# Performance work log

Hardware: AMD Instinct MI355X
Metric: run time of the kernel (lower is better)

The kernel has to match this reference:

```python
import jax, jax.numpy as jnp
import numpy as np

# SSD prior config (small VGGLite-style)
FEATURE_MAPS = [10, 5, 3, 1]
BOXES_PER_LOC = [4, 4, 4, 4]
IMG = 128      # ssd_config.DATA.SHAPE[0] -> WhereTransformer image_size
OBJ = 64
ZWHAT = 64
HID = 512
B = 4
N_OBJ = sum(f * f for f in FEATURE_MAPS)                       # 135
N_FEAT = sum(b * f * f for f, b in zip(FEATURE_MAPS, BOXES_PER_LOC))  # 540


def reconstruction_indices():
    # Replicates Decoder.reconstruction_indices: map per-location latents to per-box slots.
    idx = []
    last = 0
    for f, bpl in zip(FEATURE_MAPS, BOXES_PER_LOC):
        for i in range(f * f):
            idx.extend([last + i] * bpl)
        last += f * f
    return np.asarray(idx, dtype=np.int32)


def what_decode(z, W1, b1, W2, b2):
    # WhatDecoder: MLP z_what -> 3xOBJxOBJ object glyph in (0,1)
    h = jax.nn.relu(z @ W1 + b1)
    return jax.nn.sigmoid(h @ W2 + b2).reshape(-1, 3, OBJ, OBJ)


def where_stn(imgs, zw):
    # WhereTransformer: paste each object image into its (cx, cy, w, h) box on an IMGxIMG canvas
    # via inverse-affine bilinear sampling with zero padding (STN / grid_sample semantics).
    cx, cy, w, h = zw[:, 0], zw[:, 1], zw[:, 2], zw[:, 3]
    w = jnp.maximum(w, 1e-2)
    h = jnp.maximum(h, 1e-2)
    lin = jnp.linspace(-1.0, 1.0, IMG)
    gy, gx = jnp.meshgrid(lin, lin, indexing='ij')           # (IMG, IMG)
    u = (gx[None] - (2.0 * cx - 1.0)[:, None, None]) / w[:, None, None]
    v = (gy[None] - (2.0 * cy - 1.0)[:, None, None]) / h[:, None, None]
    px = (u + 1.0) * 0.5 * (OBJ - 1)                          # (N, IMG, IMG)
    py = (v + 1.0) * 0.5 * (OBJ - 1)

    def sample_one(img, py, px):  # img: (3, OBJ, OBJ)
        x0 = jnp.floor(px); y0 = jnp.floor(py)
        wx = px - x0; wy = py - y0
        x0i = x0.astype(jnp.int32); y0i = y0.astype(jnp.int32)

        def tap(yi, xi, wgt):
            valid = (yi >= 0) & (yi < OBJ) & (xi >= 0) & (xi < OBJ)
            yc = jnp.clip(yi, 0, OBJ - 1)
            xc = jnp.clip(xi, 0, OBJ - 1)
            return img[:, yc, xc] * (wgt * valid)[None]

        return (tap(y0i, x0i, (1 - wy) * (1 - wx)) + tap(y0i, x0i + 1, (1 - wy) * wx)
                + tap(y0i + 1, x0i, wy * (1 - wx)) + tap(y0i + 1, x0i + 1, wy * wx))

    return jax.vmap(sample_one)(imgs, py, px)                 # (N, 3, IMG, IMG)


def setup_inputs() -> dict:
    key = jax.random.key(0)
    ks = jax.random.split(key, 8)
    return {
        'z_what': jax.random.normal(ks[0], (B, N_OBJ, ZWHAT), jnp.float32),
        'z_where': jax.random.uniform(ks[1], (B, N_FEAT, 4), jnp.float32),
        'z_depth': jax.random.normal(ks[2], (B, N_OBJ, 1), jnp.float32),
        'W1': jax.random.normal(ks[3], (ZWHAT, HID), jnp.float32) * 0.05,
        'b1': jnp.zeros((HID,), jnp.float32),
        'W2': jax.random.normal(ks[4], (HID, 3 * OBJ * OBJ), jnp.float32) * 0.02,
        'b2': jnp.zeros((3 * OBJ * OBJ,), jnp.float32),
        'z_present': jax.random.randint(ks[5], (B, N_FEAT, 1), 0, 2, jnp.int32),
    }


def reference(z_what, z_where, z_depth, W1, b1, W2, b2, z_present):
    idx = jnp.asarray(reconstruction_indices())
    # index_select: replicate per-location latents across boxes-per-location
    zw_full = z_what[:, idx]                                  # (B, N_FEAT, ZWHAT)
    zd_full = z_depth[:, idx]                                 # (B, N_FEAT, 1)
    # sort descending by depth; gather all latents in that order
    order = jnp.argsort(-zd_full[..., 0], axis=1)             # (B, N_FEAT)
    s_what = jnp.take_along_axis(zw_full, order[..., None], axis=1)
    s_where = jnp.take_along_axis(z_where, order[..., None], axis=1)
    s_pres = jnp.take_along_axis(z_present, order[..., None], axis=1)
    # decode + STN warp all objects; absent objects are zeroed (equivalent to the
    dec = what_decode(s_what.reshape(-1, ZWHAT), W1, b1, W2, b2)
    warped = where_stn(dec, s_where.reshape(-1, 4))
    imgs = warped.reshape(B, N_FEAT, 3, IMG, IMG) * s_pres.astype(warped.dtype)[..., None, None]
    # depth compositing: per channel-pixel, take the first nonzero value in sorted order
    nz = imgs != 0
    first = jnp.argmax(nz, axis=1)                            # (B, 3, IMG, IMG)
    out = jnp.take_along_axis(imgs, first[:, None], axis=1)[:, 0] * nz.any(axis=1)
    return out
```

## Files before the change

### kernel.cpp

```cpp
#include <hip/hip_runtime.h>
#include <hip/hip_bf16.h>
#include <math.h>

#define NBOX  540
#define NOBJ  135
#define ZW    64
#define HIDN  512
#define NOUT  12288
#define OBJS  64
#define BATCH 4

#define ROLE_WIN   256
#define ROLE_G1    540
#define PRE_BLOCKS (ROLE_WIN + ROLE_G1)

#define G2_BLOCKS  1920

#define OFF_NROWS  0u
#define OFF_USED   256u
#define OFF_REMAP  2560u
#define OFF_ROWOBJ 4864u
#define OFF_PXWIN  7680u
#define OFF_HBF    269824u
#define OFF_DEC    13508096u

typedef short  bf16x8 __attribute__((ext_vector_type(8)));
typedef float  f32x4  __attribute__((ext_vector_type(4)));

struct F4 { float x, y, z, w; };

#define GLOAD_LDS16(gp, lp)                                                    \
  __builtin_amdgcn_global_load_lds(                                            \
      (const __attribute__((address_space(1))) void*)(gp),                     \
      (__attribute__((address_space(3))) void*)(lp), 16, 0, 0)

__device__ __forceinline__ unsigned short f2bf(float x) {
  __hip_bfloat16 h = __float2bfloat16(x);
  return *(unsigned short*)&h;
}

__global__ __launch_bounds__(256) void k_pre(
    const float* __restrict__ z_depth,
    const float* __restrict__ z_where,
    const int*   __restrict__ z_present,
    const float* __restrict__ Z,
    const float* __restrict__ W1,
    const float* __restrict__ b1,
    int* __restrict__ nrowsp,
    int* __restrict__ used,
    int* __restrict__ remap,
    int* __restrict__ rowobj,
    int* __restrict__ pxwin,
    unsigned short* __restrict__ Hbf)
{
  __shared__ union ShMem {
    struct {
      unsigned long long keys[256];
      F4       cf[NBOX];
      unsigned cbb[NBOX];
      int      cbx[NBOX];
    } win;
    float    zs[ZW];
  } u;
  __shared__ int wsums[4], woff[4], nPs;

  const int bid = blockIdx.x;
  const int t   = threadIdx.x;

  if (bid < ROLE_WIN) {
#pragma clang fp contract(off)
    const int b    = bid >> 6;
    const int tile = bid & 63;
    const int lane = t & 63, wv = t >> 6;
    const int y = (tile >> 3) * 16 + (t >> 4);
    const int x = (tile & 7) * 16 + (t & 15);

    unsigned long long key = ~0ull;
    if (t < NOBJ) {
      unsigned uu = __float_as_uint(z_depth[b * NOBJ + t]);
      uu = (uu & 0x80000000u) ? ~uu : (uu | 0x80000000u);
      key = ((unsigned long long)(~uu) << 32) | (unsigned)t;
    }
    u.win.keys[t] = key;
    __syncthreads();
    for (int k = 2; k <= 256; k <<= 1) {
      for (int j = k >> 1; j > 0; j >>= 1) {
        int ixj = t ^ j;
        if (ixj > t) {
          unsigned long long a = u.win.keys[t], c = u.win.keys[ixj];
          bool asc = (t & k) == 0;
          if (asc ? (a > c) : (a < c)) { u.win.keys[t] = c; u.win.keys[ixj] = a; }
        }
        __syncthreads();
      }
    }

    int boxq[3], presq[3], cnt = 0;
#pragma unroll
    for (int q = 0; q < 3; q++) {
      int e = 3 * t + q;
      presq[q] = 0; boxq[q] = 0;
      if (e < NBOX) {
        int o  = (int)(u.win.keys[e >> 2] & 0xFFFFFFFFull);
        int bx = o * 4 + (e & 3);
        boxq[q]  = bx;
        presq[q] = (z_present[b * NBOX + bx] != 0) ? 1 : 0;
        cnt += presq[q];
      }
    }
    int incl = cnt;
#pragma unroll
    for (int o = 1; o < 64; o <<= 1) {
      int vprev = __shfl_up(incl, o, 64);
      if (lane >= o) incl += vprev;
    }
    if (lane == 63) wsums[wv] = incl;
    __syncthreads();
    if (t == 0) {
      int a = 0;
#pragma unroll
      for (int i = 0; i < 4; i++) { woff[i] = a; a += wsums[i]; }
      nPs = a;
    }
    __syncthreads();
    int slot = woff[wv] + incl - cnt;
#pragma unroll
    for (int q = 0; q < 3; q++) {
      if (presq[q]) {
        int bx = boxq[q];
        F4 p = *(const F4*)&z_where[((size_t)b * NBOX + bx) * 4];
        double w  = fmax((double)p.z, 0.01);
        double h  = fmax((double)p.w, 0.01);
        double tx = 2.0 * (double)p.x - 1.0;
        double ty = 2.0 * (double)p.y - 1.0;
        const double S = 65.0 / 63.0;
        int xlo = (int)floor((tx - w * S + 1.0) * 63.5) - 1;
        int xhi = (int)floor((tx + w * S + 1.0) * 63.5) + 2;
        int ylo = (int)floor((ty - h * S + 1.0) * 63.5) - 1;
        int yhi = (int)floor((ty + h * S + 1.0) * 63.5) + 2;
        xlo = max(xlo, 0); ylo = max(ylo, 0);
        xhi = min(xhi, 127); yhi = min(yhi, 127);
        unsigned bb = (xhi < xlo || yhi < ylo) ? 0xFFu
                    : ((unsigned)xlo | ((unsigned)xhi << 8) |
                       ((unsigned)ylo << 16) | ((unsigned)yhi << 24));
        F4 f;
        f.x = (float)tx; f.y = (float)ty;
        f.z = (float)(w * S); f.w = (float)(h * S);
        u.win.cf[slot]  = f;
        u.win.cbb[slot] = bb;
        u.win.cbx[slot] = bx;
        slot++;
      }
    }
    __syncthreads();

    const int nP = nPs;
    const double step = 2.0 / 127.0;
    const double gx = (x == 127) ? 1.0 : ((double)x * step + (-1.0));
    const double gy = (y == 127) ? 1.0 : ((double)y * step + (-1.0));
    const float gxf = (float)gx, gyf = (float)gy;
    const int tx0 = (tile & 7) * 16, tx1 = tx0 + 15;
    const int wy0 = (tile >> 3) * 16 + wv * 4, wy1 = wy0 + 3;

    bool done = false;
    int  win  = -1;
    for (int j = 0; j < nP; j++) {
      if (__all((int)done)) break;
      unsigned bb = u.win.cbb[j];
      int bxlo = (int)(bb & 255u),         bxhi = (int)((bb >> 8) & 255u);
      int bylo = (int)((bb >> 16) & 255u), byhi = (int)(bb >> 24);
      if (bxhi < tx0 || bxlo > tx1 || byhi < wy0 || bylo > wy1) continue;
      bool newly = false;
      if (!done) {
        F4 f = u.win.cf[j];
        float dx = fabsf(gxf - f.x), dy = fabsf(gyf - f.y);
        bool in_lo = (dx < f.z * 0.9999f - 2e-6f) & (dy < f.w * 0.9999f - 2e-6f);
        bool in_hi = (dx < f.z * 1.0001f + 2e-6f) & (dy < f.w * 1.0001f + 2e-6f);
        bool cov;
        if (in_lo) {
          cov = true;
        } else if (!in_hi) {
          cov = false;
        } else {
          F4 p = *(const F4*)&z_where[((size_t)b * NBOX + u.win.cbx[j]) * 4];
          double w  = fmax((double)p.z, 0.01);
          double h  = fmax((double)p.w, 0.01);
          double tx = 2.0 * (double)p.x - 1.0;
          double ty = 2.0 * (double)p.y - 1.0;
          double uu = (gx - tx) / w;
          double vv = (gy - ty) / h;
          double px = (uu + 1.0) * 0.5 * 63.0;
          double py = (vv + 1.0) * 0.5 * 63.0;
          cov = (px > -1.0) && (px < 64.0) && (py > -1.0) && (py < 64.0);
        }
        if (cov) { win = u.win.cbx[j]; done = true; newly = true; }
      }
      unsigned long long nm = __ballot((int)newly);
      if (nm != 0ull && lane == (int)__builtin_ctzll(nm)) {
        int oi = b * NOBJ + (win >> 2);
        if (atomicCAS(&used[oi], 0, 1) == 0) {
          int rr = atomicAdd(nrowsp, 1);
          rowobj[rr] = oi;
          remap[oi]  = rr;
        }
      }
    }
    pxwin[b * 16384 + y * 128 + x] = win;
  } else {
    const int r = bid - ROLE_WIN;
    if (t < ZW) u.zs[t] = Z[(size_t)r * ZW + t];
    __syncthreads();
    float a0 = b1[t], a1 = b1[t + 256];
#pragma unroll 8
    for (int k = 0; k < ZW; k++) {
      float z = u.zs[k];
      a0 += z * W1[(size_t)k * HIDN + t];
      a1 += z * W1[(size_t)k * HIDN + t + 256];
    }
    Hbf[(size_t)r * HIDN + t]       = f2bf(fmaxf(a0, 0.f));
    Hbf[(size_t)r * HIDN + t + 256] = f2bf(fmaxf(a1, 0.f));
  }
}

__global__ __launch_bounds__(256) void k_gemm2_mfma(
    const unsigned short* __restrict__ Hbf,
    const float* __restrict__ W2,
    const float* __restrict__ b2,
    const int* __restrict__ nrowsp,
    const int* __restrict__ rowobj,
    float* __restrict__ dec)
{
  __shared__ unsigned short As[2][128 * 32];
  __shared__ float          BsF[2][32 * 32];
  const int nr = *nrowsp;
  int bid = (int)blockIdx.x;
  bid = (bid & 7) * 240 + (bid >> 3);
  const int m0 = (bid % 5) * 128;
  if (m0 >= nr) return;
  const int n0 = (bid / 5) * 32;

  const int t    = threadIdx.x;
  const int lane = t & 63, wv = t >> 6;
  const int wm = (wv & 1) * 64;
  const int wn = (wv >> 1) * 16;

  const int r0  = t >> 2;
  const int kc0 = (t & 3) ^ (r0 & 3);
  const int r1  = r0 + 64;
  const int kc1 = (t & 3) ^ (r1 & 3);

  const int ga0 = (m0 + r0 < nr) ? rowobj[m0 + r0] : 0;
  const int ga1 = (m0 + r1 < nr) ? rowobj[m0 + r1] : 0;
  const unsigned short* a0p = Hbf + (size_t)ga0 * HIDN + kc0 * 8;
  const unsigned short* a1p = Hbf + (size_t)ga1 * HIDN + kc1 * 8;
  const float* bp = W2 + (size_t)(t >> 3) * NOUT + n0 + (t & 7) * 4;

  const int fr = lane & 15;
  const int fj = lane >> 4;
  f32x4 acc[4] = {};

#define STAGE(buf, kt)                                                         \
  do {                                                                         \
    GLOAD_LDS16(a0p + (kt) * 32, &As[buf][t * 8]);                             \
    GLOAD_LDS16(a1p + (kt) * 32, &As[buf][(t + 256) * 8]);                     \
    GLOAD_LDS16(bp + (size_t)(kt) * 32 * NOUT, &BsF[buf][t * 4]);              \
  } while (0)

  STAGE(0, 0);
  __syncthreads();
  int cur = 0;
  for (int kt = 0; kt < HIDN / 32; ++kt) {
    if (kt < HIDN / 32 - 1) STAGE(cur ^ 1, kt + 1);
    bf16x8 av[4];
#pragma unroll
    for (int mi = 0; mi < 4; mi++) {
      int row = wm + mi * 16 + fr;
      av[mi] = *(const bf16x8*)&As[cur][(row * 4 + (fj ^ (row & 3))) * 8];
    }
    bf16x8 bv;
#pragma unroll
    for (int j = 0; j < 8; j++)
      bv[j] = (short)f2bf(BsF[cur][(fj * 8 + j) * 32 + wn + fr]);
#pragma unroll
    for (int mi = 0; mi < 4; mi++)
      acc[mi] = __builtin_amdgcn_mfma_f32_16x16x32_bf16(av[mi], bv, acc[mi], 0, 0, 0);
    __syncthreads();
    cur ^= 1;
  }
#undef STAGE

  const int col = n0 + wn + fr;
  const float bb = b2[col];
#pragma unroll
  for (int mi = 0; mi < 4; mi++) {
#pragma unroll
    for (int r = 0; r < 4; r++) {
      int row = m0 + wm + mi * 16 + fj * 4 + r;
      float v = acc[mi][r] + bb;
      dec[(size_t)row * NOUT + col] = 1.0f / (1.0f + __expf(-v));
    }
  }
}

__global__ __launch_bounds__(256) void k_composite(
    const int* __restrict__ pxwin, const int* __restrict__ remap,
    const float* __restrict__ z_where, const float* __restrict__ dec,
    float* __restrict__ out)
{
#pragma clang fp contract(off)
  const int bid  = blockIdx.x;
  const int t    = threadIdx.x;
  const int b    = bid >> 6;
  const int tile = bid & 63;
  const int y = (tile >> 3) * 16 + (t >> 4);
  const int x = (tile & 7) * 16 + (t & 15);

  const int win = pxwin[b * 16384 + y * 128 + x];
  float o0 = 0.f, o1 = 0.f, o2 = 0.f;
  if (win >= 0) {
    const F4 p = *(const F4*)&z_where[((size_t)b * NBOX + win) * 4];
    const double step = 2.0 / 127.0;
    const double gx = (x == 127) ? 1.0 : ((double)x * step + (-1.0));
    const double gy = (y == 127) ? 1.0 : ((double)y * step + (-1.0));
    double w = fmax((double)p.z, 0.01);
    double h = fmax((double)p.w, 0.01);
    double tx = 2.0 * (double)p.x - 1.0;
    double ty = 2.0 * (double)p.y - 1.0;
    double u = (gx - tx) / w;
    double v = (gy - ty) / h;
    double px = (u + 1.0) * 0.5 * 63.0;
    double py = (v + 1.0) * 0.5 * 63.0;
    double fx = floor(px), fy = floor(py);
    double wx = px - fx, wy = py - fy;
    int x0 = (int)fx, y0 = (int)fy;
    int x1 = x0 + 1, y1 = y0 + 1;
    bool vx0 = (x0 >= 0) && (x0 < OBJS);
    bool vx1 = (x1 >= 0) && (x1 < OBJS);
    bool vy0 = (y0 >= 0) && (y0 < OBJS);
    bool vy1 = (y1 >= 0) && (y1 < OBJS);
    double w00 = (1.0 - wy) * (1.0 - wx);
    double w01 = (1.0 - wy) * wx;
    double w10 = wy * (1.0 - wx);
    double w11 = wy * wx;
    bool c00 = vy0 && vx0 && (w00 > 0.0);
    bool c01 = vy0 && vx1 && (w01 > 0.0);
    bool c10 = vy1 && vx0 && (w10 > 0.0);
    bool c11 = vy1 && vx1 && (w11 > 0.0);
    const int row = remap[b * NOBJ + (win >> 2)];
    const float* g = dec + (size_t)row * NOUT;
    double s0 = 0.0, s1 = 0.0, s2 = 0.0;
    if (c00) { int o = y0*64 + x0; s0 += g[o]*w00; s1 += g[4096+o]*w00; s2 += g[8192+o]*w00; }
    if (c01) { int o = y0*64 + x1; s0 += g[o]*w01; s1 += g[4096+o]*w01; s2 += g[8192+o]*w01; }
    if (c10) { int o = y1*64 + x0; s0 += g[o]*w10; s1 += g[4096+o]*w10; s2 += g[8192+o]*w10; }
    if (c11) { int o = y1*64 + x1; s0 += g[o]*w11; s1 += g[4096+o]*w11; s2 += g[8192+o]*w11; }
    o0 = (float)s0; o1 = (float)s1; o2 = (float)s2;
  }
  const int ob = b * 3 * 16384 + y * 128 + x;
  out[ob]         = o0;
  out[ob + 16384] = o1;
  out[ob + 32768] = o2;
}

extern "C" void kernel_launch(void* const* d_in, const int* in_sizes, int n_in,
                              void* d_out, int out_size, void* d_ws, size_t ws_size,
                              hipStream_t stream) {
  (void)in_sizes; (void)n_in; (void)out_size; (void)ws_size;
  const float* z_what    = (const float*)d_in[0];
  const float* z_where   = (const float*)d_in[1];
  const float* z_depth   = (const float*)d_in[2];
  const float* W1        = (const float*)d_in[3];
  const float* b1        = (const float*)d_in[4];
  const float* W2        = (const float*)d_in[5];
  const float* b2        = (const float*)d_in[6];
  const int*   z_present = (const int*)d_in[7];
  float* out = (float*)d_out;
  char* ws = (char*)d_ws;

  int*            nrowsp = (int*)(ws + OFF_NROWS);
  int*            used   = (int*)(ws + OFF_USED);
  int*            remap  = (int*)(ws + OFF_REMAP);
  int*            rowobj = (int*)(ws + OFF_ROWOBJ);
  int*            pxwin  = (int*)(ws + OFF_PXWIN);
  unsigned short* Hbf    = (unsigned short*)(ws + OFF_HBF);
  float*          dec    = (float*)(ws + OFF_DEC);

  hipMemsetAsync(ws + OFF_NROWS, 0, 2560, stream);

  k_pre<<<dim3(PRE_BLOCKS), dim3(256), 0, stream>>>(
      z_depth, z_where, z_present, z_what, W1, b1,
      nrowsp, used, remap, rowobj, pxwin, Hbf);
  k_gemm2_mfma<<<dim3(G2_BLOCKS), dim3(256), 0, stream>>>(
      Hbf, W2, b2, nrowsp, rowobj, dec);
  k_composite<<<dim3(256), dim3(256), 0, stream>>>(pxwin, remap, z_where, dec, out);
}
```

Measured before the change: 118.8 us.

## Triple-buffer GEMM2 with BK=64, rank-sort depths, batch 4 rows per GEMM1 block

The second GEMM moves to a K-tile of 64 with a three-stage LDS ring, using explicit vmcnt waits and one barrier per tile so global loads overlap MFMA work across two tiles ahead. The bitonic sort of 256 keys with many barriers becomes an O(n^2) rank count that needs only two barriers. The first GEMM computes 4 rows per block instead of 1, so each W1 load is reused four times and the block count drops. These add LDS pressure and rely on hand-written waitcnt accounting.

```diff
diff --git a/kernel.cpp b/kernel.cpp
--- a/kernel.cpp
+++ b/kernel.cpp
@@ -11,10 +11,12 @@
 #define BATCH 4
 
 #define ROLE_WIN   256
-#define ROLE_G1    540
+#define ROLE_G1    135
 #define PRE_BLOCKS (ROLE_WIN + ROLE_G1)
 
 #define G2_BLOCKS  1920
+#define BK   64
+#define NK   (HIDN / BK)
 
 #define OFF_NROWS  0u
 #define OFF_USED   256u
@@ -55,12 +57,13 @@
 {
   __shared__ union ShMem {
     struct {
-      unsigned long long keys[256];
+      unsigned su[136];
+      int      sobj[136];
       F4       cf[NBOX];
       unsigned cbb[NBOX];
       int      cbx[NBOX];
     } win;
-    float    zs[ZW];
+    float    zs[4][ZW];
   } u;
   __shared__ int wsums[4], woff[4], nPs;
 
@@ -75,25 +78,22 @@
     const int y = (tile >> 3) * 16 + (t >> 4);
     const int x = (tile & 7) * 16 + (t & 15);
 
-    unsigned long long key = ~0ull;
     if (t < NOBJ) {
       unsigned uu = __float_as_uint(z_depth[b * NOBJ + t]);
       uu = (uu & 0x80000000u) ? ~uu : (uu | 0x80000000u);
-      key = ((unsigned long long)(~uu) << 32) | (unsigned)t;
-    }
-    u.win.keys[t] = key;
-    __syncthreads();
-    for (int k = 2; k <= 256; k <<= 1) {
-      for (int j = k >> 1; j > 0; j >>= 1) {
-        int ixj = t ^ j;
-        if (ixj > t) {
-          unsigned long long a = u.win.keys[t], c = u.win.keys[ixj];
-          bool asc = (t & k) == 0;
-          if (asc ? (a > c) : (a < c)) { u.win.keys[t] = c; u.win.keys[ixj] = a; }
-        }
-        __syncthreads();
-      }
-    }
+      u.win.su[t] = uu;
+    }
+    __syncthreads();
+    if (t < NOBJ) {
+      const unsigned mykey = u.win.su[t];
+      int r = 0;
+      for (int j = 0; j < NOBJ; j++) {
+        unsigned kj = u.win.su[j];
+        r += (int)((kj > mykey) || (kj == mykey && j < t));
+      }
+      u.win.sobj[r] = t;
+    }
+    __syncthreads();
 
     int boxq[3], presq[3], cnt = 0;
 #pragma unroll
@@ -101,7 +101,7 @@
       int e = 3 * t + q;
       presq[q] = 0; boxq[q] = 0;
       if (e < NBOX) {
-        int o  = (int)(u.win.keys[e >> 2] & 0xFFFFFFFFull);
+        int o  = u.win.sobj[e >> 2];
         int bx = o * 4 + (e & 3);
         boxq[q]  = bx;
         presq[q] = (z_present[b * NBOX + bx] != 0) ? 1 : 0;
@@ -207,18 +207,35 @@
     }
     pxwin[b * 16384 + y * 128 + x] = win;
   } else {
-    const int r = bid - ROLE_WIN;
-    if (t < ZW) u.zs[t] = Z[(size_t)r * ZW + t];
-    __syncthreads();
-    float a0 = b1[t], a1 = b1[t + 256];
-#pragma unroll 8
-    for (int k = 0; k < ZW; k++) {
-      float z = u.zs[k];
-      a0 += z * W1[(size_t)k * HIDN + t];
-      a1 += z * W1[(size_t)k * HIDN + t + 256];
-    }
-    Hbf[(size_t)r * HIDN + t]       = f2bf(fmaxf(a0, 0.f));
-    Hbf[(size_t)r * HIDN + t + 256] = f2bf(fmaxf(a1, 0.f));
+    const int r0 = (bid - ROLE_WIN) * 4;
+    u.zs[t >> 6][t & 63] = Z[(size_t)(r0 + (t >> 6)) * ZW + (t & 63)];
+    __syncthreads();
+    float a[4][2];
+#pragma unroll
+    for (int r = 0; r < 4; r++) { a[r][0] = b1[t]; a[r][1] = b1[t + 256]; }
+#pragma unroll
+    for (int k4 = 0; k4 < 16; k4++) {
+      float4 zq[4];
+#pragma unroll
+      for (int r = 0; r < 4; r++) zq[r] = *(const float4*)&u.zs[r][k4 * 4];
+#pragma unroll
+      for (int kk = 0; kk < 4; kk++) {
+        int k = k4 * 4 + kk;
+        float w0 = W1[(size_t)k * HIDN + t];
+        float w1 = W1[(size_t)k * HIDN + t + 256];
+#pragma unroll
+        for (int r = 0; r < 4; r++) {
+          float z = ((const float*)&zq[r])[kk];
+          a[r][0] += z * w0;
+          a[r][1] += z * w1;
+        }
+      }
+    }
+#pragma unroll
+    for (int r = 0; r < 4; r++) {
+      Hbf[(size_t)(r0 + r) * HIDN + t]       = f2bf(fmaxf(a[r][0], 0.f));
+      Hbf[(size_t)(r0 + r) * HIDN + t + 256] = f2bf(fmaxf(a[r][1], 0.f));
+    }
   }
 }
 
@@ -230,8 +247,8 @@
     const int* __restrict__ rowobj,
     float* __restrict__ dec)
 {
-  __shared__ unsigned short As[2][128 * 32];
-  __shared__ float          BsF[2][32 * 32];
+  __shared__ unsigned short As[3][128 * BK];
+  __shared__ float          BsF[3][BK * 32];
   const int nr = *nrowsp;
   int bid = (int)blockIdx.x;
   bid = (bid & 7) * 240 + (bid >> 3);
@@ -244,16 +261,21 @@
   const int wm = (wv & 1) * 64;
   const int wn = (wv >> 1) * 16;
 
-  const int r0  = t >> 2;
-  const int kc0 = (t & 3) ^ (r0 & 3);
-  const int r1  = r0 + 64;
-  const int kc1 = (t & 3) ^ (r1 & 3);
-
-  const int ga0 = (m0 + r0 < nr) ? rowobj[m0 + r0] : 0;
-  const int ga1 = (m0 + r1 < nr) ? rowobj[m0 + r1] : 0;
-  const unsigned short* a0p = Hbf + (size_t)ga0 * HIDN + kc0 * 8;
-  const unsigned short* a1p = Hbf + (size_t)ga1 * HIDN + kc1 * 8;
-  const float* bp = W2 + (size_t)(t >> 3) * NOUT + n0 + (t & 7) * 4;
+  const int arow0 = t >> 3;
+  const int kk    = t & 7;
+  int ga_[4];
+#pragma unroll
+  for (int i = 0; i < 4; i++) {
+    int row = i * 32 + arow0;
+    ga_[i] = (m0 + row < nr) ? rowobj[m0 + row] : 0;
+  }
+  const unsigned short* aSrc[4];
+#pragma unroll
+  for (int i = 0; i < 4; i++) {
+    int row = i * 32 + arow0;
+    aSrc[i] = Hbf + (size_t)ga_[i] * HIDN + (kk ^ (row & 7)) * 8;
+  }
+  const float* bSrc = W2 + (size_t)(t >> 3) * NOUT + n0 + (t & 7) * 4;
 
   const int fr = lane & 15;
   const int fj = lane >> 4;
@@ -261,31 +283,39 @@
 
 #define STAGE(buf, kt)                                                         \
   do {                                                                         \
-    GLOAD_LDS16(a0p + (kt) * 32, &As[buf][t * 8]);                             \
-    GLOAD_LDS16(a1p + (kt) * 32, &As[buf][(t + 256) * 8]);                     \
-    GLOAD_LDS16(bp + (size_t)(kt) * 32 * NOUT, &BsF[buf][t * 4]);              \
+    GLOAD_LDS16(aSrc[0] + (kt) * BK, &As[buf][(0 * 256 + t) * 8]);             \
+    GLOAD_LDS16(aSrc[1] + (kt) * BK, &As[buf][(1 * 256 + t) * 8]);             \
+    GLOAD_LDS16(aSrc[2] + (kt) * BK, &As[buf][(2 * 256 + t) * 8]);             \
+    GLOAD_LDS16(aSrc[3] + (kt) * BK, &As[buf][(3 * 256 + t) * 8]);             \
+    GLOAD_LDS16(bSrc + (size_t)((kt) * BK) * NOUT, &BsF[buf][t * 4]);          \
+    GLOAD_LDS16(bSrc + (size_t)((kt) * BK + 32) * NOUT,                        \
+                &BsF[buf][(256 + t) * 4]);                                     \
   } while (0)
 
   STAGE(0, 0);
-  __syncthreads();
-  int cur = 0;
-  for (int kt = 0; kt < HIDN / 32; ++kt) {
-    if (kt < HIDN / 32 - 1) STAGE(cur ^ 1, kt + 1);
-    bf16x8 av[4];
-#pragma unroll
-    for (int mi = 0; mi < 4; mi++) {
-      int row = wm + mi * 16 + fr;
-      av[mi] = *(const bf16x8*)&As[cur][(row * 4 + (fj ^ (row & 3))) * 8];
-    }
-    bf16x8 bv;
-#pragma unroll
-    for (int j = 0; j < 8; j++)
-      bv[j] = (short)f2bf(BsF[cur][(fj * 8 + j) * 32 + wn + fr]);
-#pragma unroll
-    for (int mi = 0; mi < 4; mi++)
-      acc[mi] = __builtin_amdgcn_mfma_f32_16x16x32_bf16(av[mi], bv, acc[mi], 0, 0, 0);
-    __syncthreads();
-    cur ^= 1;
+  STAGE(1, 1);
+#pragma unroll
+  for (int kt = 0; kt < NK; ++kt) {
+    if (kt + 1 < NK) asm volatile("s_waitcnt vmcnt(6)" ::: "memory");
+    else             asm volatile("s_waitcnt vmcnt(0)" ::: "memory");
+    __builtin_amdgcn_s_barrier();
+    __builtin_amdgcn_sched_barrier(0);
+    if (kt + 2 < NK) STAGE((kt + 2) % 3, kt + 2);
+    const int bc = kt % 3;
+#pragma unroll
+    for (int ks = 0; ks < 2; ks++) {
+      bf16x8 bv;
+#pragma unroll
+      for (int j = 0; j < 8; j++)
+        bv[j] = (short)f2bf(BsF[bc][(ks * 32 + fj * 8 + j) * 32 + wn + fr]);
+#pragma unroll
+      for (int mi = 0; mi < 4; mi++) {
+        int row = wm + mi * 16 + fr;
+        int lc  = ks * 4 + fj;
+        bf16x8 av = *(const bf16x8*)&As[bc][(row * 8 + (lc ^ (row & 7))) * 8];
+        acc[mi] = __builtin_amdgcn_mfma_f32_16x16x32_bf16(av, bv, acc[mi], 0, 0, 0);
+      }
+    }
   }
 #undef STAGE
 
```

After: 112.9 us, median of 2. 1.05x faster.
